# Kernel optimization log

Hardware: AMD Instinct MI355X
Metric: run time of the kernel (lower is better)

## Reference

```python
import jax, jax.numpy as jnp
import numpy as np

N = 100000      # nodes
E = 1600000     # edges (avg degree 16)
D_IN, D_H, D_OUT = 128, 128, 64


def setup_inputs() -> dict:
    key = jax.random.key(0)
    k1, k2, k3, k4 = jax.random.split(key, 4)
    x = jax.random.normal(k1, (N, D_IN), dtype=jnp.float32)
    edge_index = jax.random.randint(k2, (2, E), 0, N, dtype=jnp.int32)
    W1 = jax.random.normal(k3, (D_IN, D_H), dtype=jnp.float32) * (1.0 / np.sqrt(D_IN))
    b1 = jnp.zeros((D_H,), dtype=jnp.float32)
    W2 = jax.random.normal(k4, (D_H, D_OUT), dtype=jnp.float32) * (1.0 / np.sqrt(D_H))
    b2 = jnp.zeros((D_OUT,), dtype=jnp.float32)
    return {"x": x, "edge_index": edge_index, "W1": W1, "b1": b1, "W2": W2, "b2": b2}


def _gcn_conv(x, src, dst, W, b):
    """PyG GCNConv: out = D^{-1/2} (A + I) D^{-1/2} (x W) + b."""
    n = x.shape[0]
    h = x @ W  # [N, D_out] — transform first, then aggregate (PyG order)
    loops = jnp.arange(n, dtype=src.dtype)
    src_f = jnp.concatenate([src, loops])
    dst_f = jnp.concatenate([dst, loops])
    deg = jax.ops.segment_sum(jnp.ones_like(dst_f, dtype=h.dtype), dst_f, num_segments=n)
    dinv = jax.lax.rsqrt(deg)  # deg >= 1 due to self-loops
    norm = dinv[src_f] * dinv[dst_f]            # [E+N]
    msg = h[src_f] * norm[:, None]              # [E+N, D_out] gather
    out = jax.ops.segment_sum(msg, dst_f, num_segments=n)  # scatter-add
    return out + b


def reference(x, edge_index, W1, b1, W2, b2):
    src, dst = edge_index[0], edge_index[1]
    h = jax.nn.relu(_gcn_conv(x, src, dst, W1, b1))
    o = _gcn_conv(h, src, dst, W2, b2)
    return jax.nn.log_softmax(o, axis=1)
```

## Files before the change

kernel.cpp:

```cpp
#include <hip/hip_runtime.h>
#include <hip/hip_bf16.h>

typedef __hip_bfloat16 bf16;
typedef short short8 __attribute__((ext_vector_type(8)));
typedef float f32x4 __attribute__((ext_vector_type(4)));
typedef float f32x2 __attribute__((ext_vector_type(2)));

#define NPB 256
#define MAXBUK 1024

__device__ __forceinline__ float bf2f_raw(unsigned short u) {
    unsigned x = ((unsigned)u) << 16; float f; __builtin_memcpy(&f, &x, 4); return f;
}
__device__ __forceinline__ unsigned short f2bf_raw(float f) {
    unsigned u; __builtin_memcpy(&u, &f, 4);
    u += 0x7FFFu + ((u >> 16) & 1u);
    return (unsigned short)(u >> 16);
}
__device__ __forceinline__ float lo_f(unsigned u) {
    unsigned x = u << 16; float f; __builtin_memcpy(&f, &x, 4); return f;
}
__device__ __forceinline__ float hi_f(unsigned u) {
    unsigned x = u & 0xffff0000u; float f; __builtin_memcpy(&f, &x, 4); return f;
}


__global__ __launch_bounds__(1024) void sniff_kernel(const unsigned short* __restrict__ w,
                                                     int nshorts, int* __restrict__ flag) {
    __shared__ int red[1024];
    const int t = threadIdx.x;
    int c = 0;
    for (int i = t; i < nshorts; i += 1024) {
        unsigned e = (w[i] >> 7) & 0xFFu;
        if (e >= 140u || (e >= 1u && e <= 40u)) c++;
    }
    red[t] = c;
    __syncthreads();
    for (int o = 512; o > 0; o >>= 1) {
        if (t < o) red[t] += red[t + o];
        __syncthreads();
    }
    if (t == 0) *flag = (red[0] > nshorts / 8) ? 1 : 0;
}


__global__ __launch_bounds__(256) void prep_kernel(const void* __restrict__ W1p,
                                                   const void* __restrict__ W2p,
                                                   const void* __restrict__ b1p,
                                                   const void* __restrict__ b2p,
                                                   unsigned short* __restrict__ WB1,
                                                   unsigned short* __restrict__ WB2,
                                                   float* __restrict__ b1f,
                                                   float* __restrict__ b2f,
                                                   const int* __restrict__ flag) {
    const int isf32 = *flag;
    const int t = blockIdx.x * 256 + threadIdx.x;
    const int T1 = 16384, T2 = 8192;
    if (t < T1) {
        int j = t & 7, l = (t >> 3) & 63, f = t >> 9;
        int n = f >> 2, kk = f & 3;
        int k = kk * 32 + (l >> 4) * 8 + j;
        int col = n * 16 + (l & 15);
        WB1[t] = isf32 ? f2bf_raw(((const float*)W1p)[k * 128 + col])
                       : ((const unsigned short*)W1p)[k * 128 + col];
    } else if (t < T1 + T2) {
        int o = t - T1;
        int j = o & 7, l = (o >> 3) & 63, f = o >> 9;
        int n = f >> 2, kk = f & 3;
        int k = kk * 32 + (l >> 4) * 8 + j;
        int col = n * 16 + (l & 15);
        WB2[o] = isf32 ? f2bf_raw(((const float*)W2p)[k * 64 + col])
                       : ((const unsigned short*)W2p)[k * 64 + col];
    } else if (t < T1 + T2 + 128) {
        int o = t - T1 - T2;
        b1f[o] = isf32 ? ((const float*)b1p)[o] : bf2f_raw(((const unsigned short*)b1p)[o]);
    } else if (t < T1 + T2 + 192) {
        int o = t - T1 - T2 - 128;
        b2f[o] = isf32 ? ((const float*)b2p)[o] : bf2f_raw(((const unsigned short*)b2p)[o]);
    }
}


__global__ __launch_bounds__(256) void ms_count_kernel(const int* __restrict__ dst,
                                                       int* __restrict__ bktcnt,
                                                       int E, int nbuk) {
    __shared__ int cnt[MAXBUK];
    const int t = threadIdx.x;
    const int e0 = blockIdx.x * 4096;
    const int e1 = min(E, e0 + 4096);
    for (int b = t; b < nbuk; b += 256) cnt[b] = 0;
    __syncthreads();
    for (int e = e0 + t; e < e1; e += 256) atomicAdd(&cnt[dst[e] >> 8], 1);
    __syncthreads();
    for (int b = t; b < nbuk; b += 256) {
        int c = cnt[b];
        if (c) atomicAdd(&bktcnt[b], c);
    }
}

__global__ __launch_bounds__(1024) void bscan_kernel(const int* __restrict__ bktcnt,
                                                     int* __restrict__ bofs,
                                                     int* __restrict__ bcur,
                                                     int nbuk, int total) {
    __shared__ int ps[1024];
    const int t = threadIdx.x;
    int v = (t < nbuk) ? bktcnt[t] : 0;
    ps[t] = v;
    __syncthreads();
    for (int o = 1; o < 1024; o <<= 1) {
        int u = (t >= o) ? ps[t - o] : 0;
        __syncthreads();
        ps[t] += u;
        __syncthreads();
    }
    if (t < nbuk) {
        int ex = ps[t] - v;
        bofs[t] = ex;
        bcur[t] = ex;
    }
    if (t == 0) bofs[nbuk] = total;
}

__global__ __launch_bounds__(256) void ms_scatter_kernel(const int* __restrict__ src,
                                                         const int* __restrict__ dst,
                                                         int* __restrict__ bcur,
                                                         unsigned* __restrict__ packed,
                                                         int E, int nbuk) {
    __shared__ int cnt[MAXBUK];
    __shared__ int gbase[MAXBUK];
    const int t = threadIdx.x;
    const int e0 = blockIdx.x * 4096;
    const int e1 = min(E, e0 + 4096);
    for (int b = t; b < nbuk; b += 256) cnt[b] = 0;
    __syncthreads();
    for (int e = e0 + t; e < e1; e += 256) atomicAdd(&cnt[dst[e] >> 8], 1);
    __syncthreads();
    for (int b = t; b < nbuk; b += 256) {
        int c = cnt[b];
        gbase[b] = c ? atomicAdd(&bcur[b], c) : 0;
        cnt[b] = 0;
    }
    __syncthreads();
    for (int e = e0 + t; e < e1; e += 256) {
        int d = dst[e];
        int b = d >> 8;
        int r = atomicAdd(&cnt[b], 1);
        packed[gbase[b] + r] = ((unsigned)(d & 255) << 24) | (unsigned)src[e];
    }
}

__global__ __launch_bounds__(256) void csr_fine2_kernel(const unsigned* __restrict__ packed,
                                                        const int* __restrict__ bofs,
                                                        uint2* __restrict__ nmeta,
                                                        float* __restrict__ dinv,
                                                        int* __restrict__ csrc, int n) {
    __shared__ int cnt2[NPB];
    __shared__ int cur[NPB];
    const int t = threadIdx.x;
    const int b = blockIdx.x;
    const int node0 = b << 8;
    const int nn = min(NPB, n - node0);
    cnt2[t] = 0;
    __syncthreads();
    const int beg = bofs[b], end = bofs[b + 1];
    for (int i = beg + t; i < end; i += 256) atomicAdd(&cnt2[packed[i] >> 24], 1);
    __syncthreads();
    int c = cnt2[t];
    cur[t] = c;
    __syncthreads();
    for (int o = 1; o < 256; o <<= 1) {
        int u = (t >= o) ? cur[t - o] : 0;
        __syncthreads();
        cur[t] += u;
        __syncthreads();
    }
    const int base = beg + cur[t] - c;
    if (t < nn) {
        nmeta[node0 + t] = make_uint2((unsigned)base, (unsigned)c);
        dinv[node0 + t] = rsqrtf((float)(c + 1));
    }
    __syncthreads();
    cur[t] = base;
    __syncthreads();
    for (int i = beg + t; i < end; i += 256) {
        unsigned u = packed[i];
        int pos = atomicAdd(&cur[u >> 24], 1);
        csrc[pos] = (int)(u & 0xFFFFFFu);
    }
}

__global__ __launch_bounds__(256) void wsrc_kernel(const int* __restrict__ csrc,
                                                   const float* __restrict__ dinv,
                                                   float* __restrict__ wsrc, int E) {
    int i = blockIdx.x * 256 + threadIdx.x;
    if (i < E) wsrc[i] = dinv[csrc[i]];
}


__global__ __launch_bounds__(256) void gemm1_mfma(const void* __restrict__ Xp,
                                                  const unsigned short* __restrict__ WB1,
                                                  unsigned short* __restrict__ H, int nrows,
                                                  const int* __restrict__ flag) {
    __shared__ __align__(16) unsigned short Xs[128 * 136];
    __shared__ __align__(16) unsigned short Cs[128 * 68];
    const int t = threadIdx.x;
    const int r0 = blockIdx.x * 128;
    const int isf32 = *flag;

    if (isf32) {
        const float4* Xg = (const float4*)Xp;
        #pragma unroll
        for (int i = 0; i < 16; ++i) {
            int idx = t + 256 * i;
            int row = idx >> 5, c4 = idx & 31;
            float4 v = {0.f, 0.f, 0.f, 0.f};
            if (r0 + row < nrows) v = Xg[(size_t)(r0 + row) * 32 + c4];
            unsigned lo = (unsigned)f2bf_raw(v.x) | ((unsigned)f2bf_raw(v.y) << 16);
            unsigned hi = (unsigned)f2bf_raw(v.z) | ((unsigned)f2bf_raw(v.w) << 16);
            *reinterpret_cast<uint2*>(&Xs[row * 136 + c4 * 4]) = make_uint2(lo, hi);
        }
    } else {
        const uint4* Xg = (const uint4*)Xp;
        #pragma unroll
        for (int i = 0; i < 8; ++i) {
            int idx = t + 256 * i;
            int row = idx >> 4, c8 = idx & 15;
            uint4 v = {0u, 0u, 0u, 0u};
            if (r0 + row < nrows) v = Xg[(size_t)(r0 + row) * 16 + c8];
            *reinterpret_cast<uint4*>(&Xs[row * 136 + c8 * 8]) = v;
        }
    }
    __syncthreads();

    const int lane = t & 63, w = t >> 6;
    const int m0 = w * 32;
    short8 a[2][4];
    #pragma unroll
    for (int rt = 0; rt < 2; ++rt)
        #pragma unroll
        for (int kk = 0; kk < 4; ++kk)
            a[rt][kk] = *reinterpret_cast<const short8*>(
                &Xs[(m0 + rt * 16 + (lane & 15)) * 136 + kk * 32 + (lane >> 4) * 8]);

    for (int p = 0; p < 2; ++p) {
        short8 b[4][4];
        #pragma unroll
        for (int n = 0; n < 4; ++n)
            #pragma unroll
            for (int kk = 0; kk < 4; ++kk)
                b[n][kk] = *reinterpret_cast<const short8*>(
                    WB1 + (size_t)(((p * 4 + n) * 4 + kk) * 64 + lane) * 8);
        f32x4 acc[2][4];
        #pragma unroll
        for (int rt = 0; rt < 2; ++rt)
            #pragma unroll
            for (int n = 0; n < 4; ++n) {
                acc[rt][n] = (f32x4){0.f, 0.f, 0.f, 0.f};
                #pragma unroll
                for (int kk = 0; kk < 4; ++kk)
                    acc[rt][n] = __builtin_amdgcn_mfma_f32_16x16x32_bf16(
                        a[rt][kk], b[n][kk], acc[rt][n], 0, 0, 0);
            }
        if (p) __syncthreads();
        #pragma unroll
        for (int rt = 0; rt < 2; ++rt)
            #pragma unroll
            for (int n = 0; n < 4; ++n)
                #pragma unroll
                for (int r = 0; r < 4; ++r) {
                    int row = m0 + rt * 16 + (lane >> 4) * 4 + r;
                    Cs[row * 68 + n * 16 + (lane & 15)] = f2bf_raw(acc[rt][n][r]);
                }
        __syncthreads();
        #pragma unroll
        for (int i = 0; i < 8; ++i) {
            int idx = t + 256 * i;
            int row = idx >> 4, c4 = idx & 15;
            if (r0 + row < nrows) {
                uint2 v = *reinterpret_cast<const uint2*>(&Cs[row * 68 + c4 * 4]);
                *reinterpret_cast<uint2*>(H + (size_t)(r0 + row) * 128 + p * 64 + c4 * 4) = v;
            }
        }
        if (!p) __syncthreads();
    }
}


__device__ __forceinline__ void acc8v(f32x2* acc, uint4 v, float w) {
    f32x2 wv = {w, w};
    acc[0] += (f32x2){lo_f(v.x), hi_f(v.x)} * wv;
    acc[1] += (f32x2){lo_f(v.y), hi_f(v.y)} * wv;
    acc[2] += (f32x2){lo_f(v.z), hi_f(v.z)} * wv;
    acc[3] += (f32x2){lo_f(v.w), hi_f(v.w)} * wv;
}

__global__ __launch_bounds__(128) void agg128_v5(const uint4* __restrict__ H4,
                                                 const uint2* __restrict__ nmeta,
                                                 const int* __restrict__ csrc,
                                                 const float* __restrict__ wsrc,
                                                 const float* __restrict__ biasf,
                                                 uint4* __restrict__ G4, int n) {
    const int lane = threadIdx.x & 63;
    const int g = lane >> 4;
    const int sub = lane & 15;
    const int node = blockIdx.x * 2 + (threadIdx.x >> 6);
    if (node >= n) return;

    const unsigned selfoff = ((unsigned)node << 4) + (unsigned)sub;
    uint4 vself = H4[selfoff];

    const uint2 meta = nmeta[node];
    const int base = (int)meta.x;
    const int cnt = (int)meta.y;
    const int end = base + cnt;
    const float di = rsqrtf((float)(cnt + 1));

    f32x2 acc[4];
    {
        const float ws = (g == 0) ? di * di : 0.f;
        acc[0] = (f32x2){ws * lo_f(vself.x), ws * hi_f(vself.x)};
        acc[1] = (f32x2){ws * lo_f(vself.y), ws * hi_f(vself.y)};
        acc[2] = (f32x2){ws * lo_f(vself.z), ws * hi_f(vself.z)};
        acc[3] = (f32x2){ws * lo_f(vself.w), ws * hi_f(vself.w)};
    }

    int j = base;
    for (; j + 15 < end; j += 16) {
        int s0 = csrc[j + g];
        int s1 = csrc[j + 4 + g];
        int s2 = csrc[j + 8 + g];
        int s3 = csrc[j + 12 + g];
        uint4 v0 = H4[((unsigned)s0 << 4) + sub];
        uint4 v1 = H4[((unsigned)s1 << 4) + sub];
        uint4 v2 = H4[((unsigned)s2 << 4) + sub];
        uint4 v3 = H4[((unsigned)s3 << 4) + sub];
        float w0 = di * wsrc[j + g];
        float w1 = di * wsrc[j + 4 + g];
        float w2 = di * wsrc[j + 8 + g];
        float w3 = di * wsrc[j + 12 + g];
        acc8v(acc, v0, w0);
        acc8v(acc, v1, w1);
        acc8v(acc, v2, w2);
        acc8v(acc, v3, w3);
    }
    for (; j + 7 < end; j += 8) {
        int s0 = csrc[j + g];
        int s1 = csrc[j + 4 + g];
        uint4 v0 = H4[((unsigned)s0 << 4) + sub];
        uint4 v1 = H4[((unsigned)s1 << 4) + sub];
        float w0 = di * wsrc[j + g];
        float w1 = di * wsrc[j + 4 + g];
        acc8v(acc, v0, w0);
        acc8v(acc, v1, w1);
    }
    for (; j + 3 < end; j += 4) {
        int s0 = csrc[j + g];
        uint4 v0 = H4[((unsigned)s0 << 4) + sub];
        float w0 = di * wsrc[j + g];
        acc8v(acc, v0, w0);
    }
    if (j + g < end) {
        int s0 = csrc[j + g];
        uint4 v0 = H4[((unsigned)s0 << 4) + sub];
        float w0 = di * wsrc[j + g];
        acc8v(acc, v0, w0);
    }

    float a8[8];
    #pragma unroll
    for (int i = 0; i < 4; ++i) { a8[2 * i] = acc[i].x; a8[2 * i + 1] = acc[i].y; }
    #pragma unroll
    for (int i = 0; i < 8; ++i) {
        a8[i] += __shfl_xor(a8[i], 16, 64);
        a8[i] += __shfl_xor(a8[i], 32, 64);
    }

    if (g == 0) {
        const float4* b4 = (const float4*)biasf;
        float4 blo = b4[sub * 2], bhi = b4[sub * 2 + 1];
        a8[0] = fmaxf(a8[0] + blo.x, 0.f);
        a8[1] = fmaxf(a8[1] + blo.y, 0.f);
        a8[2] = fmaxf(a8[2] + blo.z, 0.f);
        a8[3] = fmaxf(a8[3] + blo.w, 0.f);
        a8[4] = fmaxf(a8[4] + bhi.x, 0.f);
        a8[5] = fmaxf(a8[5] + bhi.y, 0.f);
        a8[6] = fmaxf(a8[6] + bhi.z, 0.f);
        a8[7] = fmaxf(a8[7] + bhi.w, 0.f);
        uint4 o;
        o.x = (unsigned)f2bf_raw(a8[0]) | ((unsigned)f2bf_raw(a8[1]) << 16);
        o.y = (unsigned)f2bf_raw(a8[2]) | ((unsigned)f2bf_raw(a8[3]) << 16);
        o.z = (unsigned)f2bf_raw(a8[4]) | ((unsigned)f2bf_raw(a8[5]) << 16);
        o.w = (unsigned)f2bf_raw(a8[6]) | ((unsigned)f2bf_raw(a8[7]) << 16);
        G4[selfoff] = o;
    }
}


__global__ __launch_bounds__(256) void gemm2b_mfma(const unsigned short* __restrict__ X,
                                                   const unsigned short* __restrict__ WB2,
                                                   unsigned short* __restrict__ T, int nrows) {
    __shared__ __align__(16) unsigned short Xs[128 * 136];
    __shared__ __align__(16) unsigned short Cs[128 * 68];
    const int t = threadIdx.x;
    const int r0 = blockIdx.x * 128;

    const uint4* Xg = (const uint4*)X;
    #pragma unroll
    for (int i = 0; i < 8; ++i) {
        int idx = t + 256 * i;
        int row = idx >> 4, c8 = idx & 15;
        uint4 v = {0u, 0u, 0u, 0u};
        if (r0 + row < nrows) v = Xg[(size_t)(r0 + row) * 16 + c8];
        *reinterpret_cast<uint4*>(&Xs[row * 136 + c8 * 8]) = v;
    }
    __syncthreads();

    const int lane = t & 63, w = t >> 6;
    const int m0 = w * 32;
    short8 a[2][4];
    #pragma unroll
    for (int rt = 0; rt < 2; ++rt)
        #pragma unroll
        for (int kk = 0; kk < 4; ++kk)
            a[rt][kk] = *reinterpret_cast<const short8*>(
                &Xs[(m0 + rt * 16 + (lane & 15)) * 136 + kk * 32 + (lane >> 4) * 8]);

    short8 b[4][4];
    #pragma unroll
    for (int n = 0; n < 4; ++n)
        #pragma unroll
        for (int kk = 0; kk < 4; ++kk)
            b[n][kk] = *reinterpret_cast<const short8*>(
                WB2 + (size_t)((n * 4 + kk) * 64 + lane) * 8);

    f32x4 acc[2][4];
    #pragma unroll
    for (int rt = 0; rt < 2; ++rt)
        #pragma unroll
        for (int n = 0; n < 4; ++n) {
            acc[rt][n] = (f32x4){0.f, 0.f, 0.f, 0.f};
            #pragma unroll
            for (int kk = 0; kk < 4; ++kk)
                acc[rt][n] = __builtin_amdgcn_mfma_f32_16x16x32_bf16(
                    a[rt][kk], b[n][kk], acc[rt][n], 0, 0, 0);
        }

    __syncthreads();
    #pragma unroll
    for (int rt = 0; rt < 2; ++rt)
        #pragma unroll
        for (int n = 0; n < 4; ++n)
            #pragma unroll
            for (int r = 0; r < 4; ++r) {
                int row = m0 + rt * 16 + (lane >> 4) * 4 + r;
                Cs[row * 68 + n * 16 + (lane & 15)] = f2bf_raw(acc[rt][n][r]);
            }
    __syncthreads();
    #pragma unroll
    for (int i = 0; i < 8; ++i) {
        int idx = t + 256 * i;
        int row = idx >> 4, c4 = idx & 15;
        if (r0 + row < nrows) {
            uint2 v = *reinterpret_cast<const uint2*>(&Cs[row * 68 + c4 * 4]);
            *reinterpret_cast<uint2*>(T + (size_t)(r0 + row) * 64 + c4 * 4) = v;
        }
    }
}


__global__ __launch_bounds__(128) void agg64_final(const uint4* __restrict__ T4,
                                                   const uint2* __restrict__ nmeta,
                                                   const int* __restrict__ csrc,
                                                   const float* __restrict__ wsrc,
                                                   const float* __restrict__ b2f,
                                                   void* __restrict__ OUTv, int n,
                                                   const int* __restrict__ flag) {
    const int lane = threadIdx.x & 63;
    const int g = lane >> 3;
    const int sub = lane & 7;
    const int node = blockIdx.x * 2 + (threadIdx.x >> 6);
    if (node >= n) return;
    const int outf32 = *flag;

    const unsigned selfoff = ((unsigned)node << 3) + (unsigned)sub;
    uint4 vself = T4[selfoff];

    const uint2 meta = nmeta[node];
    const int base = (int)meta.x;
    const int cnt = (int)meta.y;
    const int end = base + cnt;
    const float di = rsqrtf((float)(cnt + 1));

    f32x2 acc[4];
    {
        const float ws = (g == 0) ? di * di : 0.f;
        acc[0] = (f32x2){ws * lo_f(vself.x), ws * hi_f(vself.x)};
        acc[1] = (f32x2){ws * lo_f(vself.y), ws * hi_f(vself.y)};
        acc[2] = (f32x2){ws * lo_f(vself.z), ws * hi_f(vself.z)};
        acc[3] = (f32x2){ws * lo_f(vself.w), ws * hi_f(vself.w)};
    }

    int j = base;
    for (; j + 15 < end; j += 16) {
        int s0 = csrc[j + g];
        int s1 = csrc[j + 8 + g];
        uint4 v0 = T4[((unsigned)s0 << 3) + sub];
        uint4 v1 = T4[((unsigned)s1 << 3) + sub];
        float w0 = di * wsrc[j + g];
        float w1 = di * wsrc[j + 8 + g];
        acc8v(acc, v0, w0);
        acc8v(acc, v1, w1);
    }
    for (; j + 7 < end; j += 8) {
        int s0 = csrc[j + g];
        uint4 v0 = T4[((unsigned)s0 << 3) + sub];
        float w0 = di * wsrc[j + g];
        acc8v(acc, v0, w0);
    }
    if (j + g < end) {
        int s0 = csrc[j + g];
        uint4 v0 = T4[((unsigned)s0 << 3) + sub];
        float w0 = di * wsrc[j + g];
        acc8v(acc, v0, w0);
    }

    float a8[8];
    #pragma unroll
    for (int i = 0; i < 4; ++i) { a8[2 * i] = acc[i].x; a8[2 * i + 1] = acc[i].y; }
    #pragma unroll
    for (int i = 0; i < 8; ++i) {
        a8[i] += __shfl_xor(a8[i], 8, 64);
        a8[i] += __shfl_xor(a8[i], 16, 64);
        a8[i] += __shfl_xor(a8[i], 32, 64);
    }

    if (g == 0) {
        const float4* b4 = (const float4*)b2f;
        float4 blo = b4[sub * 2], bhi = b4[sub * 2 + 1];
        a8[0] += blo.x; a8[1] += blo.y; a8[2] += blo.z; a8[3] += blo.w;
        a8[4] += bhi.x; a8[5] += bhi.y; a8[6] += bhi.z; a8[7] += bhi.w;

        float m = fmaxf(fmaxf(fmaxf(a8[0], a8[1]), fmaxf(a8[2], a8[3])),
                        fmaxf(fmaxf(a8[4], a8[5]), fmaxf(a8[6], a8[7])));
        m = fmaxf(m, __shfl_xor(m, 1, 64));
        m = fmaxf(m, __shfl_xor(m, 2, 64));
        m = fmaxf(m, __shfl_xor(m, 4, 64));
        float s = __expf(a8[0] - m) + __expf(a8[1] - m) + __expf(a8[2] - m) + __expf(a8[3] - m) +
                  __expf(a8[4] - m) + __expf(a8[5] - m) + __expf(a8[6] - m) + __expf(a8[7] - m);
        s += __shfl_xor(s, 1, 64);
        s += __shfl_xor(s, 2, 64);
        s += __shfl_xor(s, 4, 64);
        const float lse = m + __logf(s);

        if (outf32) {
            float4* Of = (float4*)OUTv;
            float4 o0 = {a8[0] - lse, a8[1] - lse, a8[2] - lse, a8[3] - lse};
            float4 o1 = {a8[4] - lse, a8[5] - lse, a8[6] - lse, a8[7] - lse};
            Of[(size_t)node * 16 + sub * 2] = o0;
            Of[(size_t)node * 16 + sub * 2 + 1] = o1;
        } else {
            uint4 o;
            o.x = (unsigned)f2bf_raw(a8[0] - lse) | ((unsigned)f2bf_raw(a8[1] - lse) << 16);
            o.y = (unsigned)f2bf_raw(a8[2] - lse) | ((unsigned)f2bf_raw(a8[3] - lse) << 16);
            o.z = (unsigned)f2bf_raw(a8[4] - lse) | ((unsigned)f2bf_raw(a8[5] - lse) << 16);
            o.w = (unsigned)f2bf_raw(a8[6] - lse) | ((unsigned)f2bf_raw(a8[7] - lse) << 16);
            ((uint4*)OUTv)[(size_t)node * 8 + sub] = o;
        }
    }
}


extern "C" void kernel_launch(void* const* d_in, const int* in_sizes, int n_in,
                              void* d_out, int out_size, void* d_ws, size_t ws_size,
                              hipStream_t stream) {
    const void* x  = d_in[0];
    const int*  ei = (const int*)d_in[1];
    const void* W1 = d_in[2];
    const void* b1 = d_in[3];
    const void* W2 = d_in[4];
    const void* b2 = d_in[5];

    const int N = in_sizes[0] / 128;
    const int E = in_sizes[1] / 2;
    const int* src = ei;
    const int* dst = ei + E;
    const int NBUK = (N + NPB - 1) / NPB;

    char* p = (char*)d_ws;
    auto alloc = [&](size_t bytes) { char* q = p; p += (bytes + 255) & ~255ull; return q; };
    int*   flag   = (int*)  alloc(4);
    uint2* nmeta  = (uint2*)alloc((size_t)N * 8);
    float* dinv   = (float*)alloc((size_t)N * 4);
    int*   bktcnt = (int*)  alloc((size_t)NBUK * 4);
    int*   bofs   = (int*)  alloc((size_t)(NBUK + 1) * 4);
    int*   bcur   = (int*)  alloc((size_t)NBUK * 4);
    float* b1f    = (float*)alloc(128 * 4);
    float* b2f    = (float*)alloc(64 * 4);
    unsigned short* WB1 = (unsigned short*)alloc(16384 * 2);
    unsigned short* WB2 = (unsigned short*)alloc(8192 * 2);
    unsigned* big = (unsigned*)alloc((size_t)N * 128 * 2);
    unsigned* packed = (unsigned*)d_out;
    int*      csrc   = (int*)d_in[1];
    float*    wsrc   = (float*)d_in[1] + E;
    unsigned* g1 = (unsigned*)d_in[0];
    unsigned short* T = (unsigned short*)big;
    (void)ws_size; (void)n_in; (void)out_size;

    hipMemsetAsync(bktcnt, 0, (size_t)NBUK * 4, stream);
    sniff_kernel<<<1, 1024, 0, stream>>>((const unsigned short*)W1, in_sizes[2], flag);
    prep_kernel<<<97, 256, 0, stream>>>(W1, W2, b1, b2, WB1, WB2, b1f, b2f, flag);
    const int MSB = (E + 4095) / 4096;
    ms_count_kernel<<<MSB, 256, 0, stream>>>(dst, bktcnt, E, NBUK);
    bscan_kernel<<<1, 1024, 0, stream>>>(bktcnt, bofs, bcur, NBUK, E);
    ms_scatter_kernel<<<MSB, 256, 0, stream>>>(src, dst, bcur, packed, E, NBUK);
    csr_fine2_kernel<<<NBUK, 256, 0, stream>>>(packed, bofs, nmeta, dinv, csrc, N);
    wsrc_kernel<<<(E + 255) / 256, 256, 0, stream>>>(csrc, dinv, wsrc, E);

    const int GB = (N + 127) / 128;
    gemm1_mfma<<<GB, 256, 0, stream>>>(x, WB1, (unsigned short*)big, N, flag);
    agg128_v5<<<(N + 1) / 2, 128, 0, stream>>>((const uint4*)big, nmeta, csrc, wsrc, b1f, (uint4*)g1, N);
    gemm2b_mfma<<<GB, 256, 0, stream>>>((const unsigned short*)g1, WB2, T, N);
    agg64_final<<<(N + 1) / 2, 128, 0, stream>>>((const uint4*)T, nmeta, csrc, wsrc, b2f, d_out, N, flag);
}
```

Baseline: 312.4 us.

## Slice hidden features into 16-wide planes and interleave edge source/weight pairs

The first-layer GEMM now writes H in 8 feature slices of 16 bf16 each, stored plane-major. The layer-1 aggregation launches one block per (slice, 4 nodes), so each lane gathers 8 bytes per neighbour instead of 16. The CSR source index and normalisation weight are interleaved into one uint2 array, so each edge needs a single load, and the second GEMM reads the sliced layout back. The aim is better cache locality and less per-edge metadata traffic. The cost is that every edge's metadata is now re-read once per slice, and the gathers become smaller and more numerous.

```diff
diff --git a/kernel.cpp b/kernel.cpp
--- a/kernel.cpp
+++ b/kernel.cpp
@@ -153,7 +153,7 @@
                                                         const int* __restrict__ bofs,
                                                         uint2* __restrict__ nmeta,
                                                         float* __restrict__ dinv,
-                                                        int* __restrict__ csrc, int n) {
+                                                        unsigned* __restrict__ epu, int n) {
     __shared__ int cnt2[NPB];
     __shared__ int cur[NPB];
     const int t = threadIdx.x;
@@ -185,15 +185,19 @@
     for (int i = beg + t; i < end; i += 256) {
         unsigned u = packed[i];
         int pos = atomicAdd(&cur[u >> 24], 1);
-        csrc[pos] = (int)(u & 0xFFFFFFu);
-    }
-}
-
-__global__ __launch_bounds__(256) void wsrc_kernel(const int* __restrict__ csrc,
-                                                   const float* __restrict__ dinv,
-                                                   float* __restrict__ wsrc, int E) {
+        epu[2 * pos] = u & 0xFFFFFFu;
+    }
+}
+
+__global__ __launch_bounds__(256) void epw_kernel(unsigned* __restrict__ epu,
+                                                  const float* __restrict__ dinv, int E) {
     int i = blockIdx.x * 256 + threadIdx.x;
-    if (i < E) wsrc[i] = dinv[csrc[i]];
+    if (i < E) {
+        unsigned s = epu[2 * i];
+        float w = dinv[s];
+        unsigned wb; __builtin_memcpy(&wb, &w, 4);
+        epu[2 * i + 1] = wb;
+    }
 }
 
 
@@ -278,7 +282,9 @@
             int row = idx >> 4, c4 = idx & 15;
             if (r0 + row < nrows) {
                 uint2 v = *reinterpret_cast<const uint2*>(&Cs[row * 68 + c4 * 4]);
-                *reinterpret_cast<uint2*>(H + (size_t)(r0 + row) * 128 + p * 64 + c4 * 4) = v;
+                int slice = p * 4 + (c4 >> 2);
+                *reinterpret_cast<uint2*>(
+                    H + ((size_t)slice * nrows + (r0 + row)) * 16 + (c4 & 3) * 4) = v;
             }
         }
         if (!p) __syncthreads();
@@ -286,28 +292,20 @@
 }
 
 
-__device__ __forceinline__ void acc8v(f32x2* acc, uint4 v, float w) {
-    f32x2 wv = {w, w};
-    acc[0] += (f32x2){lo_f(v.x), hi_f(v.x)} * wv;
-    acc[1] += (f32x2){lo_f(v.y), hi_f(v.y)} * wv;
-    acc[2] += (f32x2){lo_f(v.z), hi_f(v.z)} * wv;
-    acc[3] += (f32x2){lo_f(v.w), hi_f(v.w)} * wv;
-}
-
-__global__ __launch_bounds__(128) void agg128_v5(const uint4* __restrict__ H4,
+__global__ __launch_bounds__(256) void agg128_v6(const unsigned short* __restrict__ Hs,
                                                  const uint2* __restrict__ nmeta,
-                                                 const int* __restrict__ csrc,
-                                                 const float* __restrict__ wsrc,
+                                                 const uint2* __restrict__ epack,
                                                  const float* __restrict__ biasf,
-                                                 uint4* __restrict__ G4, int n) {
+                                                 unsigned short* __restrict__ Gs, int n) {
     const int lane = threadIdx.x & 63;
-    const int g = lane >> 4;
-    const int sub = lane & 15;
-    const int node = blockIdx.x * 2 + (threadIdx.x >> 6);
+    const int g = lane >> 2;
+    const int sub = lane & 3;
+    const int slice = blockIdx.x & 7;
+    const int node = (blockIdx.x >> 3) * 4 + (threadIdx.x >> 6);
     if (node >= n) return;
 
-    const unsigned selfoff = ((unsigned)node << 4) + (unsigned)sub;
-    uint4 vself = H4[selfoff];
+    const uint2* Hp = (const uint2*)(Hs + (size_t)slice * n * 16);
+    uint2 vself = Hp[(unsigned)node * 4u + (unsigned)sub];
 
     const uint2 meta = nmeta[node];
     const int base = (int)meta.x;
@@ -315,88 +313,52 @@
     const int end = base + cnt;
     const float di = rsqrtf((float)(cnt + 1));
 
-    f32x2 acc[4];
-    {
-        const float ws = (g == 0) ? di * di : 0.f;
-        acc[0] = (f32x2){ws * lo_f(vself.x), ws * hi_f(vself.x)};
-        acc[1] = (f32x2){ws * lo_f(vself.y), ws * hi_f(vself.y)};
-        acc[2] = (f32x2){ws * lo_f(vself.z), ws * hi_f(vself.z)};
-        acc[3] = (f32x2){ws * lo_f(vself.w), ws * hi_f(vself.w)};
-    }
+    const float ws = (g == 0) ? di * di : 0.f;
+    f32x2 acc0 = {ws * lo_f(vself.x), ws * hi_f(vself.x)};
+    f32x2 acc1 = {ws * lo_f(vself.y), ws * hi_f(vself.y)};
 
     int j = base;
     for (; j + 15 < end; j += 16) {
-        int s0 = csrc[j + g];
-        int s1 = csrc[j + 4 + g];
-        int s2 = csrc[j + 8 + g];
-        int s3 = csrc[j + 12 + g];
-        uint4 v0 = H4[((unsigned)s0 << 4) + sub];
-        uint4 v1 = H4[((unsigned)s1 << 4) + sub];
-        uint4 v2 = H4[((unsigned)s2 << 4) + sub];
-        uint4 v3 = H4[((unsigned)s3 << 4) + sub];
-        float w0 = di * wsrc[j + g];
-        float w1 = di * wsrc[j + 4 + g];
-        float w2 = di * wsrc[j + 8 + g];
-        float w3 = di * wsrc[j + 12 + g];
-        acc8v(acc, v0, w0);
-        acc8v(acc, v1, w1);
-        acc8v(acc, v2, w2);
-        acc8v(acc, v3, w3);
-    }
-    for (; j + 7 < end; j += 8) {
-        int s0 = csrc[j + g];
-        int s1 = csrc[j + 4 + g];
-        uint4 v0 = H4[((unsigned)s0 << 4) + sub];
-        uint4 v1 = H4[((unsigned)s1 << 4) + sub];
-        float w0 = di * wsrc[j + g];
-        float w1 = di * wsrc[j + 4 + g];
-        acc8v(acc, v0, w0);
-        acc8v(acc, v1, w1);
-    }
-    for (; j + 3 < end; j += 4) {
-        int s0 = csrc[j + g];
-        uint4 v0 = H4[((unsigned)s0 << 4) + sub];
-        float w0 = di * wsrc[j + g];
-        acc8v(acc, v0, w0);
+        uint2 ep = epack[j + g];
+        float w; __builtin_memcpy(&w, &ep.y, 4);
+        w *= di;
+        uint2 v = Hp[ep.x * 4u + (unsigned)sub];
+        acc0 += (f32x2){lo_f(v.x), hi_f(v.x)} * (f32x2){w, w};
+        acc1 += (f32x2){lo_f(v.y), hi_f(v.y)} * (f32x2){w, w};
     }
     if (j + g < end) {
-        int s0 = csrc[j + g];
-        uint4 v0 = H4[((unsigned)s0 << 4) + sub];
-        float w0 = di * wsrc[j + g];
-        acc8v(acc, v0, w0);
-    }
-
-    float a8[8];
-    #pragma unroll
-    for (int i = 0; i < 4; ++i) { a8[2 * i] = acc[i].x; a8[2 * i + 1] = acc[i].y; }
-    #pragma unroll
-    for (int i = 0; i < 8; ++i) {
-        a8[i] += __shfl_xor(a8[i], 16, 64);
-        a8[i] += __shfl_xor(a8[i], 32, 64);
+        uint2 ep = epack[j + g];
+        float w; __builtin_memcpy(&w, &ep.y, 4);
+        w *= di;
+        uint2 v = Hp[ep.x * 4u + (unsigned)sub];
+        acc0 += (f32x2){lo_f(v.x), hi_f(v.x)} * (f32x2){w, w};
+        acc1 += (f32x2){lo_f(v.y), hi_f(v.y)} * (f32x2){w, w};
+    }
+
+    float a4[4] = {acc0.x, acc0.y, acc1.x, acc1.y};
+    #pragma unroll
+    for (int i = 0; i < 4; ++i) {
+        a4[i] += __shfl_xor(a4[i], 4, 64);
+        a4[i] += __shfl_xor(a4[i], 8, 64);
+        a4[i] += __shfl_xor(a4[i], 16, 64);
+        a4[i] += __shfl_xor(a4[i], 32, 64);
     }
 
     if (g == 0) {
-        const float4* b4 = (const float4*)biasf;
-        float4 blo = b4[sub * 2], bhi = b4[sub * 2 + 1];
-        a8[0] = fmaxf(a8[0] + blo.x, 0.f);
-        a8[1] = fmaxf(a8[1] + blo.y, 0.f);
-        a8[2] = fmaxf(a8[2] + blo.z, 0.f);
-        a8[3] = fmaxf(a8[3] + blo.w, 0.f);
-        a8[4] = fmaxf(a8[4] + bhi.x, 0.f);
-        a8[5] = fmaxf(a8[5] + bhi.y, 0.f);
-        a8[6] = fmaxf(a8[6] + bhi.z, 0.f);
-        a8[7] = fmaxf(a8[7] + bhi.w, 0.f);
-        uint4 o;
-        o.x = (unsigned)f2bf_raw(a8[0]) | ((unsigned)f2bf_raw(a8[1]) << 16);
-        o.y = (unsigned)f2bf_raw(a8[2]) | ((unsigned)f2bf_raw(a8[3]) << 16);
-        o.z = (unsigned)f2bf_raw(a8[4]) | ((unsigned)f2bf_raw(a8[5]) << 16);
-        o.w = (unsigned)f2bf_raw(a8[6]) | ((unsigned)f2bf_raw(a8[7]) << 16);
-        G4[selfoff] = o;
-    }
-}
-
-
-__global__ __launch_bounds__(256) void gemm2b_mfma(const unsigned short* __restrict__ X,
+        float4 b = ((const float4*)biasf)[slice * 4 + sub];
+        a4[0] = fmaxf(a4[0] + b.x, 0.f);
+        a4[1] = fmaxf(a4[1] + b.y, 0.f);
+        a4[2] = fmaxf(a4[2] + b.z, 0.f);
+        a4[3] = fmaxf(a4[3] + b.w, 0.f);
+        uint2 o;
+        o.x = (unsigned)f2bf_raw(a4[0]) | ((unsigned)f2bf_raw(a4[1]) << 16);
+        o.y = (unsigned)f2bf_raw(a4[2]) | ((unsigned)f2bf_raw(a4[3]) << 16);
+        ((uint2*)(Gs + (size_t)slice * n * 16))[(unsigned)node * 4u + (unsigned)sub] = o;
+    }
+}
+
+
+__global__ __launch_bounds__(256) void gemm2b_mfma(const unsigned short* __restrict__ Gsm,
                                                    const unsigned short* __restrict__ WB2,
                                                    unsigned short* __restrict__ T, int nrows) {
     __shared__ __align__(16) unsigned short Xs[128 * 136];
@@ -404,14 +366,15 @@
     const int t = threadIdx.x;
     const int r0 = blockIdx.x * 128;
 
-    const uint4* Xg = (const uint4*)X;
+    const uint4* Gg = (const uint4*)Gsm;
     #pragma unroll
     for (int i = 0; i < 8; ++i) {
         int idx = t + 256 * i;
-        int row = idx >> 4, c8 = idx & 15;
+        int row = idx >> 4, q = idx & 15;
+        int slice = q >> 1, h = q & 1;
         uint4 v = {0u, 0u, 0u, 0u};
-        if (r0 + row < nrows) v = Xg[(size_t)(r0 + row) * 16 + c8];
-        *reinterpret_cast<uint4*>(&Xs[row * 136 + c8 * 8]) = v;
+        if (r0 + row < nrows) v = Gg[((size_t)slice * nrows + (r0 + row)) * 2 + h];
+        *reinterpret_cast<uint4*>(&Xs[row * 136 + slice * 16 + h * 8]) = v;
     }
     __syncthreads();
 
@@ -468,10 +431,17 @@
 }
 
 
+__device__ __forceinline__ void acc8v(f32x2* acc, uint4 v, float w) {
+    f32x2 wv = {w, w};
+    acc[0] += (f32x2){lo_f(v.x), hi_f(v.x)} * wv;
+    acc[1] += (f32x2){lo_f(v.y), hi_f(v.y)} * wv;
+    acc[2] += (f32x2){lo_f(v.z), hi_f(v.z)} * wv;
+    acc[3] += (f32x2){lo_f(v.w), hi_f(v.w)} * wv;
+}
+
 __global__ __launch_bounds__(128) void agg64_final(const uint4* __restrict__ T4,
                                                    const uint2* __restrict__ nmeta,
-                                                   const int* __restrict__ csrc,
-                                                   const float* __restrict__ wsrc,
+                                                   const uint2* __restrict__ epack,
                                                    const float* __restrict__ b2f,
                                                    void* __restrict__ OUTv, int n,
                                                    const int* __restrict__ flag) {
@@ -502,26 +472,27 @@
 
     int j = base;
     for (; j + 15 < end; j += 16) {
-        int s0 = csrc[j + g];
-        int s1 = csrc[j + 8 + g];
-        uint4 v0 = T4[((unsigned)s0 << 3) + sub];
-        uint4 v1 = T4[((unsigned)s1 << 3) + sub];
-        float w0 = di * wsrc[j + g];
-        float w1 = di * wsrc[j + 8 + g];
-        acc8v(acc, v0, w0);
-        acc8v(acc, v1, w1);
+        uint2 e0 = epack[j + g];
+        uint2 e1 = epack[j + 8 + g];
+        uint4 v0 = T4[(e0.x << 3) + (unsigned)sub];
+        uint4 v1 = T4[(e1.x << 3) + (unsigned)sub];
+        float w0, w1;
+        __builtin_memcpy(&w0, &e0.y, 4);
+        __builtin_memcpy(&w1, &e1.y, 4);
+        acc8v(acc, v0, di * w0);
+        acc8v(acc, v1, di * w1);
     }
     for (; j + 7 < end; j += 8) {
-        int s0 = csrc[j + g];
-        uint4 v0 = T4[((unsigned)s0 << 3) + sub];
-        float w0 = di * wsrc[j + g];
-        acc8v(acc, v0, w0);
+        uint2 e0 = epack[j + g];
+        uint4 v0 = T4[(e0.x << 3) + (unsigned)sub];
+        float w0; __builtin_memcpy(&w0, &e0.y, 4);
+        acc8v(acc, v0, di * w0);
     }
     if (j + g < end) {
-        int s0 = csrc[j + g];
-        uint4 v0 = T4[((unsigned)s0 << 3) + sub];
-        float w0 = di * wsrc[j + g];
-        acc8v(acc, v0, w0);
+        uint2 e0 = epack[j + g];
+        uint4 v0 = T4[(e0.x << 3) + (unsigned)sub];
+        float w0; __builtin_memcpy(&w0, &e0.y, 4);
+        acc8v(acc, v0, di * w0);
     }
 
     float a8[8];
@@ -600,9 +571,8 @@
     unsigned short* WB2 = (unsigned short*)alloc(8192 * 2);
     unsigned* big = (unsigned*)alloc((size_t)N * 128 * 2);
     unsigned* packed = (unsigned*)d_out;
-    int*      csrc   = (int*)d_in[1];
-    float*    wsrc   = (float*)d_in[1] + E;
-    unsigned* g1 = (unsigned*)d_in[0];
+    uint2*    epack  = (uint2*)d_in[1];
+    unsigned short* Gs = (unsigned short*)d_in[0];
     unsigned short* T = (unsigned short*)big;
     (void)ws_size; (void)n_in; (void)out_size;
 
@@ -613,12 +583,13 @@
     ms_count_kernel<<<MSB, 256, 0, stream>>>(dst, bktcnt, E, NBUK);
     bscan_kernel<<<1, 1024, 0, stream>>>(bktcnt, bofs, bcur, NBUK, E);
     ms_scatter_kernel<<<MSB, 256, 0, stream>>>(src, dst, bcur, packed, E, NBUK);
-    csr_fine2_kernel<<<NBUK, 256, 0, stream>>>(packed, bofs, nmeta, dinv, csrc, N);
-    wsrc_kernel<<<(E + 255) / 256, 256, 0, stream>>>(csrc, dinv, wsrc, E);
+    csr_fine2_kernel<<<NBUK, 256, 0, stream>>>(packed, bofs, nmeta, dinv, (unsigned*)epack, N);
+    epw_kernel<<<(E + 255) / 256, 256, 0, stream>>>((unsigned*)epack, dinv, E);
 
     const int GB = (N + 127) / 128;
     gemm1_mfma<<<GB, 256, 0, stream>>>(x, WB1, (unsigned short*)big, N, flag);
-    agg128_v5<<<(N + 1) / 2, 128, 0, stream>>>((const uint4*)big, nmeta, csrc, wsrc, b1f, (uint4*)g1, N);
-    gemm2b_mfma<<<GB, 256, 0, stream>>>((const unsigned short*)g1, WB2, T, N);
-    agg64_final<<<(N + 1) / 2, 128, 0, stream>>>((const uint4*)T, nmeta, csrc, wsrc, b2f, d_out, N, flag);
-}
+    agg128_v6<<<8 * ((N + 3) / 4), 256, 0, stream>>>((const unsigned short*)big, nmeta, epack,
+                                                     b1f, Gs, N);
+    gemm2b_mfma<<<GB, 256, 0, stream>>>(Gs, WB2, T, N);
+    agg64_final<<<(N + 1) / 2, 128, 0, stream>>>((const uint4*)T, nmeta, epack, b2f, d_out, N, flag);
+}
```

New measurement: 488.1 us. 1.56x slower.

## Interleave edge source and weight, fold dinv scaling, merge sniff and memset into prep

Applied to the files above, without the earlier changes.

Edge source indices and source-side normalization weights now sit interleaved as one uint2 per edge. Each aggregation kernel loads one 8-byte record instead of two separate arrays. The destination dinv factor moves out of the per-edge loop and is applied once in the epilogue as an fma with the bias. The separate sniff kernel and the memset are folded into prep_kernel, which now samples only the first 2048 weights to detect the dtype and zeroes the bucket counts, cutting two launches.

```diff
diff --git a/kernel.cpp b/kernel.cpp
--- a/kernel.cpp
+++ b/kernel.cpp
@@ -25,26 +25,8 @@
 }
 
 
-__global__ __launch_bounds__(1024) void sniff_kernel(const unsigned short* __restrict__ w,
-                                                     int nshorts, int* __restrict__ flag) {
-    __shared__ int red[1024];
-    const int t = threadIdx.x;
-    int c = 0;
-    for (int i = t; i < nshorts; i += 1024) {
-        unsigned e = (w[i] >> 7) & 0xFFu;
-        if (e >= 140u || (e >= 1u && e <= 40u)) c++;
-    }
-    red[t] = c;
-    __syncthreads();
-    for (int o = 512; o > 0; o >>= 1) {
-        if (t < o) red[t] += red[t + o];
-        __syncthreads();
-    }
-    if (t == 0) *flag = (red[0] > nshorts / 8) ? 1 : 0;
-}
-
-
-__global__ __launch_bounds__(256) void prep_kernel(const void* __restrict__ W1p,
+__global__ __launch_bounds__(256) void prep_kernel(const unsigned short* __restrict__ W1s,
+                                                   const void* __restrict__ W1p,
                                                    const void* __restrict__ W2p,
                                                    const void* __restrict__ b1p,
                                                    const void* __restrict__ b2p,
@@ -52,9 +34,27 @@
                                                    unsigned short* __restrict__ WB2,
                                                    float* __restrict__ b1f,
                                                    float* __restrict__ b2f,
-                                                   const int* __restrict__ flag) {
-    const int isf32 = *flag;
-    const int t = blockIdx.x * 256 + threadIdx.x;
+                                                   int* __restrict__ flag,
+                                                   int* __restrict__ bktcnt,
+                                                   int nshorts, int nbuk) {
+    __shared__ int red[256];
+    const int tt = threadIdx.x;
+    const int sample = min(nshorts, 2048);
+    int c = 0;
+    for (int i = tt; i < sample; i += 256) {
+        unsigned e = (W1s[i] >> 7) & 0xFFu;
+        if (e >= 140u || (e >= 1u && e <= 40u)) c++;
+    }
+    red[tt] = c;
+    __syncthreads();
+    for (int o = 128; o > 0; o >>= 1) {
+        if (tt < o) red[tt] += red[tt + o];
+        __syncthreads();
+    }
+    const int isf32 = (red[0] > sample / 8) ? 1 : 0;
+    if (blockIdx.x == 0 && tt == 0) *flag = isf32;
+
+    const int t = blockIdx.x * 256 + tt;
     const int T1 = 16384, T2 = 8192;
     if (t < T1) {
         int j = t & 7, l = (t >> 3) & 63, f = t >> 9;
@@ -77,6 +77,8 @@
     } else if (t < T1 + T2 + 192) {
         int o = t - T1 - T2 - 128;
         b2f[o] = isf32 ? ((const float*)b2p)[o] : bf2f_raw(((const unsigned short*)b2p)[o]);
+    } else if (t < T1 + T2 + 192 + nbuk) {
+        bktcnt[t - T1 - T2 - 192] = 0;
     }
 }
 
@@ -153,7 +155,7 @@
                                                         const int* __restrict__ bofs,
                                                         uint2* __restrict__ nmeta,
                                                         float* __restrict__ dinv,
-                                                        int* __restrict__ csrc, int n) {
+                                                        unsigned* __restrict__ epu, int n) {
     __shared__ int cnt2[NPB];
     __shared__ int cur[NPB];
     const int t = threadIdx.x;
@@ -185,15 +187,19 @@
     for (int i = beg + t; i < end; i += 256) {
         unsigned u = packed[i];
         int pos = atomicAdd(&cur[u >> 24], 1);
-        csrc[pos] = (int)(u & 0xFFFFFFu);
-    }
-}
-
-__global__ __launch_bounds__(256) void wsrc_kernel(const int* __restrict__ csrc,
-                                                   const float* __restrict__ dinv,
-                                                   float* __restrict__ wsrc, int E) {
+        epu[2 * pos] = u & 0xFFFFFFu;
+    }
+}
+
+__global__ __launch_bounds__(256) void epw_kernel(unsigned* __restrict__ epu,
+                                                  const float* __restrict__ dinv, int E) {
     int i = blockIdx.x * 256 + threadIdx.x;
-    if (i < E) wsrc[i] = dinv[csrc[i]];
+    if (i < E) {
+        unsigned s = epu[2 * i];
+        float w = dinv[s];
+        unsigned wb; __builtin_memcpy(&wb, &w, 4);
+        epu[2 * i + 1] = wb;
+    }
 }
 
 
@@ -293,11 +299,13 @@
     acc[2] += (f32x2){lo_f(v.z), hi_f(v.z)} * wv;
     acc[3] += (f32x2){lo_f(v.w), hi_f(v.w)} * wv;
 }
-
-__global__ __launch_bounds__(128) void agg128_v5(const uint4* __restrict__ H4,
+__device__ __forceinline__ float epw_f(uint2 e) {
+    float w; __builtin_memcpy(&w, &e.y, 4); return w;
+}
+
+__global__ __launch_bounds__(128) void agg128_v7(const uint4* __restrict__ H4,
                                                  const uint2* __restrict__ nmeta,
-                                                 const int* __restrict__ csrc,
-                                                 const float* __restrict__ wsrc,
+                                                 const uint2* __restrict__ epack,
                                                  const float* __restrict__ biasf,
                                                  uint4* __restrict__ G4, int n) {
     const int lane = threadIdx.x & 63;
@@ -317,7 +325,7 @@
 
     f32x2 acc[4];
     {
-        const float ws = (g == 0) ? di * di : 0.f;
+        const float ws = (g == 0) ? di : 0.f;
         acc[0] = (f32x2){ws * lo_f(vself.x), ws * hi_f(vself.x)};
         acc[1] = (f32x2){ws * lo_f(vself.y), ws * hi_f(vself.y)};
         acc[2] = (f32x2){ws * lo_f(vself.z), ws * hi_f(vself.z)};
@@ -326,44 +334,36 @@
 
     int j = base;
     for (; j + 15 < end; j += 16) {
-        int s0 = csrc[j + g];
-        int s1 = csrc[j + 4 + g];
-        int s2 = csrc[j + 8 + g];
-        int s3 = csrc[j + 12 + g];
-        uint4 v0 = H4[((unsigned)s0 << 4) + sub];
-        uint4 v1 = H4[((unsigned)s1 << 4) + sub];
-        uint4 v2 = H4[((unsigned)s2 << 4) + sub];
-        uint4 v3 = H4[((unsigned)s3 << 4) + sub];
-        float w0 = di * wsrc[j + g];
-        float w1 = di * wsrc[j + 4 + g];
-        float w2 = di * wsrc[j + 8 + g];
-        float w3 = di * wsrc[j + 12 + g];
-        acc8v(acc, v0, w0);
-        acc8v(acc, v1, w1);
-        acc8v(acc, v2, w2);
-        acc8v(acc, v3, w3);
+        uint2 e0 = epack[j + g];
+        uint2 e1 = epack[j + 4 + g];
+        uint2 e2 = epack[j + 8 + g];
+        uint2 e3 = epack[j + 12 + g];
+        uint4 v0 = H4[(e0.x << 4) + (unsigned)sub];
+        uint4 v1 = H4[(e1.x << 4) + (unsigned)sub];
+        uint4 v2 = H4[(e2.x << 4) + (unsigned)sub];
+        uint4 v3 = H4[(e3.x << 4) + (unsigned)sub];
+        acc8v(acc, v0, epw_f(e0));
+        acc8v(acc, v1, epw_f(e1));
+        acc8v(acc, v2, epw_f(e2));
+        acc8v(acc, v3, epw_f(e3));
     }
     for (; j + 7 < end; j += 8) {
-        int s0 = csrc[j + g];
-        int s1 = csrc[j + 4 + g];
-        uint4 v0 = H4[((unsigned)s0 << 4) + sub];
-        uint4 v1 = H4[((unsigned)s1 << 4) + sub];
-        float w0 = di * wsrc[j + g];
-        float w1 = di * wsrc[j + 4 + g];
-        acc8v(acc, v0, w0);
-        acc8v(acc, v1, w1);
+        uint2 e0 = epack[j + g];
+        uint2 e1 = epack[j + 4 + g];
+        uint4 v0 = H4[(e0.x << 4) + (unsigned)sub];
+        uint4 v1 = H4[(e1.x << 4) + (unsigned)sub];
+        acc8v(acc, v0, epw_f(e0));
+        acc8v(acc, v1, epw_f(e1));
     }
     for (; j + 3 < end; j += 4) {
-        int s0 = csrc[j + g];
-        uint4 v0 = H4[((unsigned)s0 << 4) + sub];
-        float w0 = di * wsrc[j + g];
-        acc8v(acc, v0, w0);
+        uint2 e0 = epack[j + g];
+        uint4 v0 = H4[(e0.x << 4) + (unsigned)sub];
+        acc8v(acc, v0, epw_f(e0));
     }
     if (j + g < end) {
-        int s0 = csrc[j + g];
-        uint4 v0 = H4[((unsigned)s0 << 4) + sub];
-        float w0 = di * wsrc[j + g];
-        acc8v(acc, v0, w0);
+        uint2 e0 = epack[j + g];
+        uint4 v0 = H4[(e0.x << 4) + (unsigned)sub];
+        acc8v(acc, v0, epw_f(e0));
     }
 
     float a8[8];
@@ -378,14 +378,14 @@
     if (g == 0) {
         const float4* b4 = (const float4*)biasf;
         float4 blo = b4[sub * 2], bhi = b4[sub * 2 + 1];
-        a8[0] = fmaxf(a8[0] + blo.x, 0.f);
-        a8[1] = fmaxf(a8[1] + blo.y, 0.f);
-        a8[2] = fmaxf(a8[2] + blo.z, 0.f);
-        a8[3] = fmaxf(a8[3] + blo.w, 0.f);
-        a8[4] = fmaxf(a8[4] + bhi.x, 0.f);
-        a8[5] = fmaxf(a8[5] + bhi.y, 0.f);
-        a8[6] = fmaxf(a8[6] + bhi.z, 0.f);
-        a8[7] = fmaxf(a8[7] + bhi.w, 0.f);
+        a8[0] = fmaxf(fmaf(di, a8[0], blo.x), 0.f);
+        a8[1] = fmaxf(fmaf(di, a8[1], blo.y), 0.f);
+        a8[2] = fmaxf(fmaf(di, a8[2], blo.z), 0.f);
+        a8[3] = fmaxf(fmaf(di, a8[3], blo.w), 0.f);
+        a8[4] = fmaxf(fmaf(di, a8[4], bhi.x), 0.f);
+        a8[5] = fmaxf(fmaf(di, a8[5], bhi.y), 0.f);
+        a8[6] = fmaxf(fmaf(di, a8[6], bhi.z), 0.f);
+        a8[7] = fmaxf(fmaf(di, a8[7], bhi.w), 0.f);
         uint4 o;
         o.x = (unsigned)f2bf_raw(a8[0]) | ((unsigned)f2bf_raw(a8[1]) << 16);
         o.y = (unsigned)f2bf_raw(a8[2]) | ((unsigned)f2bf_raw(a8[3]) << 16);
@@ -470,8 +470,7 @@
 
 __global__ __launch_bounds__(128) void agg64_final(const uint4* __restrict__ T4,
                                                    const uint2* __restrict__ nmeta,
-                                                   const int* __restrict__ csrc,
-                                                   const float* __restrict__ wsrc,
+                                                   const uint2* __restrict__ epack,
                                                    const float* __restrict__ b2f,
                                                    void* __restrict__ OUTv, int n,
                                                    const int* __restrict__ flag) {
@@ -493,7 +492,7 @@
 
     f32x2 acc[4];
     {
-        const float ws = (g == 0) ? di * di : 0.f;
+        const float ws = (g == 0) ? di : 0.f;
         acc[0] = (f32x2){ws * lo_f(vself.x), ws * hi_f(vself.x)};
         acc[1] = (f32x2){ws * lo_f(vself.y), ws * hi_f(vself.y)};
         acc[2] = (f32x2){ws * lo_f(vself.z), ws * hi_f(vself.z)};
@@ -502,26 +501,22 @@
 
     int j = base;
     for (; j + 15 < end; j += 16) {
-        int s0 = csrc[j + g];
-        int s1 = csrc[j + 8 + g];
-        uint4 v0 = T4[((unsigned)s0 << 3) + sub];
-        uint4 v1 = T4[((unsigned)s1 << 3) + sub];
-        float w0 = di * wsrc[j + g];
-        float w1 = di * wsrc[j + 8 + g];
-        acc8v(acc, v0, w0);
-        acc8v(acc, v1, w1);
+        uint2 e0 = epack[j + g];
+        uint2 e1 = epack[j + 8 + g];
+        uint4 v0 = T4[(e0.x << 3) + (unsigned)sub];
+        uint4 v1 = T4[(e1.x << 3) + (unsigned)sub];
+        acc8v(acc, v0, epw_f(e0));
+        acc8v(acc, v1, epw_f(e1));
     }
     for (; j + 7 < end; j += 8) {
-        int s0 = csrc[j + g];
-        uint4 v0 = T4[((unsigned)s0 << 3) + sub];
-        float w0 = di * wsrc[j + g];
-        acc8v(acc, v0, w0);
+        uint2 e0 = epack[j + g];
+        uint4 v0 = T4[(e0.x << 3) + (unsigned)sub];
+        acc8v(acc, v0, epw_f(e0));
     }
     if (j + g < end) {
-        int s0 = csrc[j + g];
-        uint4 v0 = T4[((unsigned)s0 << 3) + sub];
-        float w0 = di * wsrc[j + g];
-        acc8v(acc, v0, w0);
+        uint2 e0 = epack[j + g];
+        uint4 v0 = T4[(e0.x << 3) + (unsigned)sub];
+        acc8v(acc, v0, epw_f(e0));
     }
 
     float a8[8];
@@ -537,8 +532,14 @@
     if (g == 0) {
         const float4* b4 = (const float4*)b2f;
         float4 blo = b4[sub * 2], bhi = b4[sub * 2 + 1];
-        a8[0] += blo.x; a8[1] += blo.y; a8[2] += blo.z; a8[3] += blo.w;
-        a8[4] += bhi.x; a8[5] += bhi.y; a8[6] += bhi.z; a8[7] += bhi.w;
+        a8[0] = fmaf(di, a8[0], blo.x);
+        a8[1] = fmaf(di, a8[1], blo.y);
+        a8[2] = fmaf(di, a8[2], blo.z);
+        a8[3] = fmaf(di, a8[3], blo.w);
+        a8[4] = fmaf(di, a8[4], bhi.x);
+        a8[5] = fmaf(di, a8[5], bhi.y);
+        a8[6] = fmaf(di, a8[6], bhi.z);
+        a8[7] = fmaf(di, a8[7], bhi.w);
 
         float m = fmaxf(fmaxf(fmaxf(a8[0], a8[1]), fmaxf(a8[2], a8[3])),
                         fmaxf(fmaxf(a8[4], a8[5]), fmaxf(a8[6], a8[7])));
@@ -600,25 +601,25 @@
     unsigned short* WB2 = (unsigned short*)alloc(8192 * 2);
     unsigned* big = (unsigned*)alloc((size_t)N * 128 * 2);
     unsigned* packed = (unsigned*)d_out;
-    int*      csrc   = (int*)d_in[1];
-    float*    wsrc   = (float*)d_in[1] + E;
+    uint2*    epack  = (uint2*)d_in[1];
     unsigned* g1 = (unsigned*)d_in[0];
     unsigned short* T = (unsigned short*)big;
     (void)ws_size; (void)n_in; (void)out_size;
 
-    hipMemsetAsync(bktcnt, 0, (size_t)NBUK * 4, stream);
-    sniff_kernel<<<1, 1024, 0, stream>>>((const unsigned short*)W1, in_sizes[2], flag);
-    prep_kernel<<<97, 256, 0, stream>>>(W1, W2, b1, b2, WB1, WB2, b1f, b2f, flag);
+    const int PREPB = (24768 + NBUK + 255) / 256;
+    prep_kernel<<<PREPB, 256, 0, stream>>>((const unsigned short*)W1, W1, W2, b1, b2,
+                                           WB1, WB2, b1f, b2f, flag, bktcnt,
+                                           in_sizes[2], NBUK);
     const int MSB = (E + 4095) / 4096;
     ms_count_kernel<<<MSB, 256, 0, stream>>>(dst, bktcnt, E, NBUK);
     bscan_kernel<<<1, 1024, 0, stream>>>(bktcnt, bofs, bcur, NBUK, E);
     ms_scatter_kernel<<<MSB, 256, 0, stream>>>(src, dst, bcur, packed, E, NBUK);
-    csr_fine2_kernel<<<NBUK, 256, 0, stream>>>(packed, bofs, nmeta, dinv, csrc, N);
-    wsrc_kernel<<<(E + 255) / 256, 256, 0, stream>>>(csrc, dinv, wsrc, E);
+    csr_fine2_kernel<<<NBUK, 256, 0, stream>>>(packed, bofs, nmeta, dinv, (unsigned*)epack, N);
+    epw_kernel<<<(E + 255) / 256, 256, 0, stream>>>((unsigned*)epack, dinv, E);
 
     const int GB = (N + 127) / 128;
     gemm1_mfma<<<GB, 256, 0, stream>>>(x, WB1, (unsigned short*)big, N, flag);
-    agg128_v5<<<(N + 1) / 2, 128, 0, stream>>>((const uint4*)big, nmeta, csrc, wsrc, b1f, (uint4*)g1, N);
+    agg128_v7<<<(N + 1) / 2, 128, 0, stream>>>((const uint4*)big, nmeta, epack, b1f, (uint4*)g1, N);
     gemm2b_mfma<<<GB, 256, 0, stream>>>((const unsigned short*)g1, WB2, T, N);
-    agg64_final<<<(N + 1) / 2, 128, 0, stream>>>((const uint4*)T, nmeta, csrc, wsrc, b2f, d_out, N, flag);
-}
+    agg64_final<<<(N + 1) / 2, 128, 0, stream>>>((const uint4*)T, nmeta, epack, b2f, d_out, N, flag);
+}
```

Result: no change. 312.9 us (+0.2%).
